# Kernel tuning notes

Hardware: AMD Instinct MI355X
Metric: run time of the kernel (lower is better)

Reference implementation:

```python
import jax, jax.numpy as jnp
import numpy as np

NUM_CLASSES = 1024
DEPTH = 10  # num_edges; complete binary tree over 2**DEPTH leaves
BATCH = 4096


def _build_tree_buffers(C=NUM_CLASSES, D=DEPTH):
    """Replicates HierarchicalLLLoss.__init__ for a complete binary hierarchy.
    onehot_num[i, :, j] = indicator of leaves under leaf i's ancestor j levels up.
    onehot_den[i, :, j] = indicator one level further up; last column is all-ones.
    weights[i, j]       = edge weight at level j (deterministic exp decay).
    """
    ids = np.arange(C)
    onehot_num = np.zeros((C, C, D), dtype=np.float32)
    onehot_den = np.zeros((C, C, D), dtype=np.float32)
    for j in range(D):
        blk = 2 ** j
        onehot_num[:, :, j] = (ids[:, None] // blk == ids[None, :] // blk)
        if j < D - 1:
            blk2 = 2 ** (j + 1)
            onehot_den[:, :, j] = (ids[:, None] // blk2 == ids[None, :] // blk2)
    onehot_den[:, :, D - 1] = 1.0
    weights = np.tile(np.exp(-0.5 * np.arange(D, dtype=np.float32))[None, :], (C, 1))
    return onehot_num, onehot_den, weights


def setup_inputs() -> dict:
    key = jax.random.key(0)
    k1, k2 = jax.random.split(key)
    # class probabilities: uniform then normalized per row
    logits = jax.random.uniform(k1, (BATCH, NUM_CLASSES), dtype=jnp.float32) + 1e-3
    inputs = logits / jnp.sum(logits, axis=1, keepdims=True)
    target = jax.random.randint(k2, (BATCH,), 0, NUM_CLASSES, dtype=jnp.int64)
    onehot_num, onehot_den, weights = _build_tree_buffers()
    return {
        "inputs": inputs,
        "target": target,
        "onehot_num": jnp.asarray(onehot_num),
        "onehot_den": jnp.asarray(onehot_den),
        "weights": jnp.asarray(weights),
    }


def reference(inputs, target, onehot_num, onehot_den, weights):
    # gather per-sample onehot trees: [B, C, E]
    oh_num = onehot_num[target]
    oh_den = onehot_den[target]
    num = jnp.einsum('bc,bce->be', inputs, oh_num)
    den = jnp.einsum('bc,bce->be', inputs, oh_den)
    idx = num != 0
    safe_num = jnp.where(idx, num, 1.0)
    safe_den = jnp.where(idx, den, 1.0)
    # where num==0, torch leaves num (==0) untouched
    val = jnp.where(idx, -jnp.log(safe_num / safe_den), num)
    # torch.flip along dim=1 is a no-op under the subsequent sum over dim=1
    per_sample = jnp.sum(weights[target] * val, axis=1)  # [B]
    return jnp.mean(per_sample)
```

## Files before the change

### kernel.cpp

```cpp
#include <hip/hip_runtime.h>

#define BATCH 4096
#define NCLS  1024
#define DEPTH 10

__global__ __launch_bounds__(256) void hll_per_sample(
    const float* __restrict__ inputs,
    const int*   __restrict__ target,
    const float* __restrict__ weights,
    float*       __restrict__ per_sample)
{
    const int wave = threadIdx.x >> 6;
    const int lane = threadIdx.x & 63;
    const int b = blockIdx.x * 4 + wave;

    const int t = target[b];
    const float4* row = reinterpret_cast<const float4*>(inputs + (size_t)b * NCLS);

    float4 x0 = row[lane * 4 + 0];
    float4 x1 = row[lane * 4 + 1];
    float4 x2 = row[lane * 4 + 2];
    float4 x3 = row[lane * 4 + 3];

    const int s = t & 15;
    const int q = s >> 2;
    const int r = s & 3;

    float4 xq = (q == 0) ? x0 : (q == 1) ? x1 : (q == 2) ? x2 : x3;

    float S[DEPTH + 1];
    S[0] = (r == 0) ? xq.x : (r == 1) ? xq.y : (r == 2) ? xq.z : xq.w;
    S[1] = (r < 2) ? (xq.x + xq.y) : (xq.z + xq.w);
    S[2] = xq.x + xq.y + xq.z + xq.w;

    const float q0 = x0.x + x0.y + x0.z + x0.w;
    const float q1 = x1.x + x1.y + x1.z + x1.w;
    const float q2 = x2.x + x2.y + x2.z + x2.w;
    const float q3 = x3.x + x3.y + x3.z + x3.w;
    S[3] = (q < 2) ? (q0 + q1) : (q2 + q3);
    S[4] = q0 + q1 + q2 + q3;

    float ssum = S[4];
    #pragma unroll
    for (int k = 0; k < 6; ++k) {
        ssum += __shfl_xor(ssum, 1 << k, 64);
        S[5 + k] = ssum;
    }

    const float* w = weights + (size_t)t * DEPTH;

    float acc = 0.0f;
    #pragma unroll
    for (int j = 0; j < DEPTH; ++j) {
        const float num = S[j];
        const float den = S[j + 1];
        const float val = (num != 0.0f) ? -__logf(num / den) : num;
        acc += w[j] * val;
    }

    if (lane == (t >> 4)) per_sample[b] = acc;
}

__global__ __launch_bounds__(256) void hll_reduce(
    const float* __restrict__ per_sample,
    float*       __restrict__ out)
{
    __shared__ float lds[256];
    const int tid = threadIdx.x;
    float s = 0.0f;
    #pragma unroll
    for (int i = 0; i < BATCH / 256; ++i)
        s += per_sample[tid + i * 256];
    lds[tid] = s;
    __syncthreads();
    #pragma unroll
    for (int off = 128; off > 0; off >>= 1) {
        if (tid < off) lds[tid] += lds[tid + off];
        __syncthreads();
    }
    if (tid == 0) out[0] = lds[0] * (1.0f / (float)BATCH);
}

extern "C" void kernel_launch(void* const* d_in, const int* in_sizes, int n_in,
                              void* d_out, int out_size, void* d_ws, size_t ws_size,
                              hipStream_t stream) {
    const float* inputs  = (const float*)d_in[0];
    const int*   target  = (const int*)d_in[1];
    const float* weights = (const float*)d_in[4];

    float* ws_per_sample = (float*)d_ws;
    float* out = (float*)d_out;

    hll_per_sample<<<BATCH / 4, 256, 0, stream>>>(inputs, target, weights, ws_per_sample);
    hll_reduce<<<1, 256, 0, stream>>>(ws_per_sample, out);
}
```

Before: 11.89 us.

## Fuse per-sample loss and mean reduction with last-block atomic counter

Merges the per-sample kernel and the separate reduction kernel into one kernel. Each block writes a block partial and bumps an atomic counter, and the last block to finish reduces all partials and writes the mean. This removes the second kernel launch and the global per-sample round trip. In exchange it adds a memset of the counter before each launch, plus a threadfence and an atomic per block.

```diff
diff --git a/kernel.cpp b/kernel.cpp
--- a/kernel.cpp
+++ b/kernel.cpp
@@ -3,12 +3,15 @@
 #define BATCH 4096
 #define NCLS  1024
 #define DEPTH 10
+#define NBLOCKS (BATCH / 4)
 
-__global__ __launch_bounds__(256) void hll_per_sample(
+__global__ __launch_bounds__(256) void hll_fused(
     const float* __restrict__ inputs,
     const int*   __restrict__ target,
     const float* __restrict__ weights,
-    float*       __restrict__ per_sample)
+    float*       __restrict__ partials,
+    unsigned int* __restrict__ counter,
+    float*       __restrict__ out)
 {
     const int wave = threadIdx.x >> 6;
     const int lane = threadIdx.x & 63;
@@ -58,27 +61,38 @@
         acc += w[j] * val;
     }
 
-    if (lane == (t >> 4)) per_sample[b] = acc;
-}
+    const float loss = __shfl(acc, t >> 4, 64);
 
-__global__ __launch_bounds__(256) void hll_reduce(
-    const float* __restrict__ per_sample,
-    float*       __restrict__ out)
-{
-    __shared__ float lds[256];
-    const int tid = threadIdx.x;
-    float s = 0.0f;
-    #pragma unroll
-    for (int i = 0; i < BATCH / 256; ++i)
-        s += per_sample[tid + i * 256];
-    lds[tid] = s;
+    __shared__ float wsum[4];
+    __shared__ int   is_last;
+    if (lane == 0) wsum[wave] = loss;
     __syncthreads();
-    #pragma unroll
-    for (int off = 128; off > 0; off >>= 1) {
-        if (tid < off) lds[tid] += lds[tid + off];
+
+    if (threadIdx.x == 0) {
+        partials[blockIdx.x] = wsum[0] + wsum[1] + wsum[2] + wsum[3];
+        __threadfence();
+        unsigned int old = atomicAdd(counter, 1u);
+        is_last = (old == NBLOCKS - 1);
+    }
+    __syncthreads();
+
+    if (is_last) {
+        __threadfence();
+        const int tid = threadIdx.x;
+        float sum = 0.0f;
+        #pragma unroll
+        for (int i = 0; i < NBLOCKS / 256; ++i)
+            sum += ((volatile const float*)partials)[tid + i * 256];
+        __shared__ float lds[256];
+        lds[tid] = sum;
         __syncthreads();
+        #pragma unroll
+        for (int off = 128; off > 0; off >>= 1) {
+            if (tid < off) lds[tid] += lds[tid + off];
+            __syncthreads();
+        }
+        if (tid == 0) out[0] = lds[0] * (1.0f / (float)BATCH);
     }
-    if (tid == 0) out[0] = lds[0] * (1.0f / (float)BATCH);
 }
 
 extern "C" void kernel_launch(void* const* d_in, const int* in_sizes, int n_in,
@@ -88,9 +102,12 @@
     const int*   target  = (const int*)d_in[1];
     const float* weights = (const float*)d_in[4];
 
-    float* ws_per_sample = (float*)d_ws;
-    float* out = (float*)d_out;
+    float*        partials = (float*)d_ws;
+    unsigned int* counter  = (unsigned int*)((char*)d_ws + 8192);
+    float*        out      = (float*)d_out;
 
-    hll_per_sample<<<BATCH / 4, 256, 0, stream>>>(inputs, target, weights, ws_per_sample);
-    hll_reduce<<<1, 256, 0, stream>>>(ws_per_sample, out);
+    hipMemsetAsync(counter, 0, sizeof(unsigned int), stream);
+
+    hll_fused<<<NBLOCKS, 256, 0, stream>>>(inputs, target, weights,
+                                           partials, counter, out);
 }
```

After: 33.58 us. 182% more time.
